# Kernel tuning notes

Hardware: AMD Instinct MI355X
Metric: run time of the kernel (lower is better)

## Reference

```python
import jax, jax.numpy as jnp
import numpy as np

N = 16384
K = 8

def knn_indices(pos, k):
    # squared pairwise distances via ||a||^2 + ||b||^2 - 2 a.b  -> [N, N]
    sq = jnp.sum(pos * pos, axis=-1)
    d = sq[:, None] + sq[None, :] - 2.0 * (pos @ pos.T)
    n = pos.shape[0]
    d = d.at[jnp.arange(n), jnp.arange(n)].set(jnp.inf)  # exclude self (loop=False)
    _, idx = jax.lax.top_k(-d, k)  # k nearest neighbors per target node
    # PointNetConv adds self-loops by default -> append self index
    return jnp.concatenate([idx, jnp.arange(n)[:, None]], axis=1)  # [N, k+1]

def mlp(x, W1, b1, W2, b2):
    return jax.nn.relu(x @ W1 + b1) @ W2 + b2

def pointnet_conv(x, pos, idx, W1, b1, W2, b2):
    # message: concat(x_j, pos_j - pos_i); aggregate: max over neighbors
    rel = pos[idx] - pos[:, None, :]                 # [N, k+1, 3]
    msg = jnp.concatenate([x[idx], rel], axis=-1)    # [N, k+1, d+3]
    h = mlp(msg, W1, b1, W2, b2)                     # [N, k+1, d_out]
    return jnp.max(h, axis=1)                        # [N, d_out]

def setup_inputs() -> dict:
    key = jax.random.key(0)
    ks = jax.random.split(key, 11)
    def lin(k, fi, fo):
        kw, kb = jax.random.split(k)
        s = 1.0 / np.sqrt(fi)
        return (jax.random.uniform(kw, (fi, fo), jnp.float32, -s, s),
                jax.random.uniform(kb, (fo,), jnp.float32, -s, s))
    W1a, b1a = lin(ks[0], 6, 32)
    W1b, b1b = lin(ks[1], 32, 64)
    W2a, b2a = lin(ks[2], 67, 64)
    W2b, b2b = lin(ks[3], 64, 128)
    Wc, bc = lin(ks[4], 128, 5)
    pos = jax.random.normal(ks[5], (N, 3), jnp.float32)
    return {"pos": pos, "W1a": W1a, "b1a": b1a, "W1b": W1b, "b1b": b1b,
            "W2a": W2a, "b2a": b2a, "W2b": W2b, "b2b": b2b, "Wc": Wc, "bc": bc}

def reference(pos, W1a, b1a, W1b, b1b, W2a, b2a, W2b, b2b, Wc, bc):
    idx = knn_indices(pos, K)                                    # [N, K+1]
    x = jax.nn.relu(pointnet_conv(pos, pos, idx, W1a, b1a, W1b, b1b))  # [N, 64]
    x = jax.nn.relu(pointnet_conv(x, pos, idx, W2a, b2a, W2b, b2b))    # [N, 128]
    logits = x @ Wc + bc                                         # [N, 5]
    return jax.nn.log_softmax(logits, axis=-1)
```

## Files before the change

kernel.cpp:

```cpp
#include <hip/hip_runtime.h>
#include <hip/hip_bf16.h>
#include <math.h>

#define N_PTS 16384
#define KNN 8

#define DT_BF16 1
#define DT_FP32 2

#define WS_FLAG_OFF 0
#define WS_IDX_OFF  64
#define WS_X1_OFF   589888
#define WS_NEEDED   4784192

#define WS_SAT_OFF      (WS_X1_OFF)
#define WS_START_OFF    (WS_X1_OFF + 442368)
#define WS_CURSOR_OFF   (WS_X1_OFF + 884800)
#define WS_PID_OFF      (WS_X1_OFF + 1327168)
#define WS_PTS_OFF      (WS_X1_OFF + 1392704)
#define WS_ROWTOT_OFF   (WS_X1_OFF + 1654848)
#define WS_ROWSTART_OFF (WS_X1_OFF + 1664064)
#define WS_XPRE_OFF     (WS_X1_OFF + 1673280)

#define GRID_R   48
#define NROWS2D  (GRID_R * GRID_R)
#define NCELLS   (GRID_R * GRID_R * GRID_R)
#define GLO      -4.5f
#define CELL_E   0.1875f
#define CELL_INV 5.3333335f
#define NBR_MIN  26
#define NBR_LO   9
#define M_CAP    768

__device__ __forceinline__ float bf2f(__hip_bfloat16 v) { return __bfloat162float(v); }

__device__ __forceinline__ float ldf(const float* p, int i) { return p[i]; }
__device__ __forceinline__ float ldf(const __hip_bfloat16* p, int i) { return bf2f(p[i]); }
__device__ __forceinline__ void stf(float* p, int i, float v) { p[i] = v; }
__device__ __forceinline__ void stf(__hip_bfloat16* p, int i, float v) { p[i] = __float2bfloat16(v); }

__device__ __forceinline__ int clamp_idx(int j) {
    return ((unsigned)j < (unsigned)N_PTS) ? j : 0;
}

__device__ __forceinline__ int cell_of(float v) {
    int c = (int)((v - GLO) * CELL_INV);
    return min(max(c, 0), GRID_R - 1);
}

__device__ __forceinline__ int get_dt(const int* flag) {
    return (flag[0] > 16) ? DT_FP32 : DT_BF16;
}

__global__ __launch_bounds__(256) void zero_kernel(int* __restrict__ cnt, int* __restrict__ flag) {
    const int e = blockIdx.x * 256 + threadIdx.x;
    cnt[e] = 0;
    if (e == 0) flag[0] = 0;
}

__global__ __launch_bounds__(256) void sniff_kernel(const unsigned short* __restrict__ posu,
                                                    int* __restrict__ flag) {
    __shared__ int red[256];
    int local = 0;
    for (int e = blockIdx.x * 256 + threadIdx.x; e < 3 * N_PTS; e += 64 * 256) {
        const float v = __uint_as_float(((unsigned)posu[e]) << 16);
        if (!(fabsf(v) <= 64.0f)) local++;
    }
    red[threadIdx.x] = local;
    __syncthreads();
    for (int s = 128; s > 0; s >>= 1) {
        if (threadIdx.x < s) red[threadIdx.x] += red[threadIdx.x + s];
        __syncthreads();
    }
    if (threadIdx.x == 0 && red[0] > 0) atomicAdd(flag, red[0]);
}

template <typename T>
__device__ __forceinline__ void count_body(const T* __restrict__ pos, int* __restrict__ cnt) {
    const int i = blockIdx.x * 256 + threadIdx.x;
    const float x = ldf(pos, 3 * i + 0);
    const float y = ldf(pos, 3 * i + 1);
    const float z = ldf(pos, 3 * i + 2);
    const int c = (cell_of(z) * GRID_R + cell_of(y)) * GRID_R + cell_of(x);
    atomicAdd(&cnt[c], 1);
}

__global__ __launch_bounds__(256) void grid_count_kernel(const void* __restrict__ pos,
                                                         const int* __restrict__ flag,
                                                         int* __restrict__ cnt) {
    if (get_dt(flag) == DT_BF16) count_body<__hip_bfloat16>((const __hip_bfloat16*)pos, cnt);
    else                         count_body<float>((const float*)pos, cnt);
}

__global__ __launch_bounds__(256) void rowscan_kernel(int* __restrict__ sat,
                                                      int* __restrict__ xpre,
                                                      int* __restrict__ rowtot) {
    const int t = blockIdx.x * 256 + threadIdx.x;
    const int rb = t * GRID_R;
    int acc = 0;
    for (int x = 0; x < GRID_R; ++x) {
        acc += sat[rb + x];
        sat[rb + x]  = acc;
        xpre[rb + x] = acc;
    }
    rowtot[t] = acc;
}

__global__ __launch_bounds__(256) void rowoffset_kernel(const int* __restrict__ rowtot,
                                                        int* __restrict__ rowstart) {
    __shared__ int part[256];
    const int t = threadIdx.x;
    int loc[9]; int s = 0;
#pragma unroll
    for (int k = 0; k < 9; ++k) { loc[k] = rowtot[t * 9 + k]; s += loc[k]; }
    part[t] = s;
    __syncthreads();
    for (int off = 1; off < 256; off <<= 1) {
        int v = (t >= off) ? part[t - off] : 0;
        __syncthreads();
        part[t] += v;
        __syncthreads();
    }
    int run = (t == 0) ? 0 : part[t - 1];
#pragma unroll
    for (int k = 0; k < 9; ++k) { rowstart[t * 9 + k] = run; run += loc[k]; }
}

__global__ __launch_bounds__(256) void cellsaty_kernel(const int* __restrict__ xpre,
                                                       const int* __restrict__ rowstart,
                                                       int* __restrict__ cstart,
                                                       int* __restrict__ cursor,
                                                       int* __restrict__ sat) {
    const int t = blockIdx.x * 256 + threadIdx.x;
    const int rb = t * GRID_R;
    const int base = rowstart[t];
    int prev = 0;
    for (int x = 0; x < GRID_R; ++x) {
        const int v = base + prev;
        cstart[rb + x] = v;
        cursor[rb + x] = v;
        prev = xpre[rb + x];
    }
    if (t == NROWS2D - 1) cstart[NCELLS] = base + prev;
    const int z = t / GRID_R, x = t - z * GRID_R;
    const int b2 = z * NROWS2D + x;
    int run = 0;
#pragma unroll
    for (int y = 0; y < GRID_R; ++y) {
        run += sat[b2 + y * GRID_R];
        sat[b2 + y * GRID_R] = run;
    }
}

template <typename T>
__device__ __forceinline__ void scatter_body(const T* __restrict__ pos, int i,
                                             int* __restrict__ cursor,
                                             float4* __restrict__ pts4, int* __restrict__ pid) {
    const float x = ldf(pos, 3 * i + 0);
    const float y = ldf(pos, 3 * i + 1);
    const float z = ldf(pos, 3 * i + 2);
    const int c = (cell_of(z) * GRID_R + cell_of(y)) * GRID_R + cell_of(x);
    const int slot = atomicAdd(&cursor[c], 1);
    const float sq = fmaf(x, x, fmaf(y, y, z * z));
    pts4[slot] = make_float4(-2.0f * x, -2.0f * y, -2.0f * z, sq);
    pid[slot] = i;
}

__global__ __launch_bounds__(256) void satzscatter_kernel(const void* __restrict__ pos,
                                                          const int* __restrict__ flag,
                                                          int* __restrict__ sat,
                                                          int* __restrict__ cursor,
                                                          float4* __restrict__ pts4,
                                                          int* __restrict__ pid) {
    if (blockIdx.x < 9) {
        const int t = blockIdx.x * 256 + threadIdx.x;
        int run = 0;
#pragma unroll
        for (int z = 0; z < GRID_R; ++z) {
            run += sat[t + z * NROWS2D];
            sat[t + z * NROWS2D] = run;
        }
    } else {
        const int i = (blockIdx.x - 9) * 256 + threadIdx.x;
        if (get_dt(flag) == DT_BF16) scatter_body<__hip_bfloat16>((const __hip_bfloat16*)pos, i, cursor, pts4, pid);
        else                         scatter_body<float>((const float*)pos, i, cursor, pts4, pid);
    }
}

__device__ __forceinline__ int sat_at(const int* __restrict__ sat, int x, int y, int z) {
    if (x < 0 || y < 0 || z < 0) return 0;
    return sat[(z * GRID_R + y) * GRID_R + x];
}

__device__ __forceinline__ int boxcount(const int* __restrict__ sat,
                                        int x0, int x1, int y0, int y1, int z0, int z1) {
    return sat_at(sat, x1, y1, z1) - sat_at(sat, x0 - 1, y1, z1)
         - sat_at(sat, x1, y0 - 1, z1) - sat_at(sat, x1, y1, z0 - 1)
         + sat_at(sat, x0 - 1, y0 - 1, z1) + sat_at(sat, x0 - 1, y1, z0 - 1)
         + sat_at(sat, x1, y0 - 1, z0 - 1) - sat_at(sat, x0 - 1, y0 - 1, z0 - 1);
}

template <typename T>
__device__ void knn_body(const T* __restrict__ pos,
                         const int* __restrict__ cstart, const int* __restrict__ sat,
                         const float4* __restrict__ pts4, const int* __restrict__ pid,
                         int* __restrict__ idx_out,
                         int* __restrict__ rs, int* __restrict__ epf) {
    const int tid  = threadIdx.x;
    const int lane = tid & 31;
    const int i    = blockIdx.x * 8 + (tid >> 5);

    const float pix = ldf(pos, 3 * i + 0);
    const float piy = ldf(pos, 3 * i + 1);
    const float piz = ldf(pos, 3 * i + 2);
    const float sqi = fmaf(pix, pix, fmaf(piy, piy, piz * piz));
    const int cx = cell_of(pix), cy = cell_of(piy), cz = cell_of(piz);

    float bd[KNN];
    int   bi[KNN];
#pragma unroll
    for (int q = 0; q < KNN; ++q) { bd[q] = INFINITY; bi[q] = 0x7fffffff; }
    float tau = INFINITY;

    auto do_insert = [&](float d, int pj) {
        float cd = d; int ci = pj;
#pragma unroll
        for (int q = 0; q < KNN; ++q) {
            const bool ins = (cd < bd[q]) || (cd == bd[q] && ci < bi[q]);
            const float nd = ins ? cd : bd[q];
            const int   ni = ins ? ci : bi[q];
            const float od = ins ? bd[q] : cd;
            const int   oi = ins ? bi[q] : ci;
            bd[q] = nd; bi[q] = ni; cd = od; ci = oi;
        }
        tau = fminf(tau, bd[KNN - 1]);
    };

    auto scan_win = [&](int rr) {
        const int x0 = max(cx - rr, 0), x1 = min(cx + rr, GRID_R - 1);
        const int y0 = max(cy - rr, 0), y1 = min(cy + rr, GRID_R - 1);
        const int z0 = max(cz - rr, 0), z1 = min(cz + rr, GRID_R - 1);
        const int ny = y1 - y0 + 1;
        const int R  = ny * (z1 - z0 + 1);
        const int xs = x1 - x0 + 1;
        for (int cb = 0; cb < R; cb += 32) {
            const int lr = cb + lane;
            int cnt_r = 0, st_r = 0;
            if (lr < R) {
                const int iz = lr / ny;
                const int iy = lr - iz * ny;
                const int c0 = ((z0 + iz) * GRID_R + (y0 + iy)) * GRID_R + x0;
                st_r  = cstart[c0];
                cnt_r = cstart[c0 + xs] - st_r;
            }
            int pv = cnt_r;
#pragma unroll
            for (int s = 1; s < 32; s <<= 1) {
                const int u = __shfl_up(pv, s, 32);
                if (lane >= s) pv += u;
            }
            const int Mtot = __shfl(pv, 31, 32);
            asm volatile("s_waitcnt lgkmcnt(0)" ::: "memory");
            rs[lane]  = st_r;
            epf[lane] = (lr < R) ? (pv - cnt_r) : 0x7fffffff;
            asm volatile("s_waitcnt lgkmcnt(0)" ::: "memory");
            for (int tb = 0; tb < Mtot; tb += 128) {
                float dls[4]; int pjs[4];
#pragma unroll
                for (int k = 0; k < 4; ++k) {
                    const int t = tb + (k << 5) + lane;
                    dls[k] = INFINITY; pjs[k] = i;
                    if (t < Mtot) {
                        int p = 0;
#pragma unroll
                        for (int st = 16; st >= 1; st >>= 1)
                            if (epf[p + st] <= t) p += st;
                        const int si = rs[p] + (t - epf[p]);
                        const float4 cq = pts4[si];
                        pjs[k] = pid[si];
                        dls[k] = fmaf(cq.x, pix, fmaf(cq.y, piy, fmaf(cq.z, piz, cq.w)));
                    }
                }
#pragma unroll
                for (int k = 0; k < 4; ++k)
                    if (pjs[k] != i && dls[k] <= tau) do_insert(dls[k], pjs[k]);
            }
        }
    };

    float od[KNN];
    int   oi[KNN];
    auto merge_out = [&]() {
#pragma unroll
        for (int k = 0; k < KNN; ++k) {
            float dw = bd[0];
            int   iw = bi[0];
#pragma unroll
            for (int s = 1; s < 32; s <<= 1) {
                const float dx = __shfl_xor(dw, s, 32);
                const int   ix = __shfl_xor(iw, s, 32);
                if (dx < dw || (dx == dw && ix < iw)) { dw = dx; iw = ix; }
            }
            if (bd[0] == dw && bi[0] == iw) {
#pragma unroll
                for (int q = 0; q < KNN - 1; ++q) { bd[q] = bd[q + 1]; bi[q] = bi[q + 1]; }
                bd[KNN - 1] = INFINITY; bi[KNN - 1] = 0x7fffffff;
            }
            od[k] = dw; oi[k] = iw;
        }
    };

    int r;
    {
        const int rl = lane + 1;
        const int bx0 = max(cx - rl, 0), bx1 = min(cx + rl, GRID_R - 1);
        const int by0 = max(cy - rl, 0), by1 = min(cy + rl, GRID_R - 1);
        const int bz0 = max(cz - rl, 0), bz1 = min(cz + rl, GRID_R - 1);
        const int cntl = boxcount(sat, bx0, bx1, by0, by1, bz0, bz1);
        const unsigned long long m9  = __ballot(cntl >= NBR_LO);
        const unsigned long long m26 = __ballot(cntl >= NBR_MIN);
        const unsigned sh  = (unsigned)(tid & 32);
        const unsigned mh9  = (unsigned)(m9  >> sh);
        const unsigned mh26 = (unsigned)(m26 >> sh);
        const int r9  = mh9  ? (int)__ffs(mh9)  : 32;
        const int r26 = mh26 ? (int)__ffs(mh26) : 32;
        const int cnt26 = __shfl(cntl, r26 - 1, 32);
        r = (cnt26 <= M_CAP) ? r26 : r9;
    }

    scan_win(r);

    {
        float mg = INFINITY;
        bool full = true;
        if (cx - r > 0)          { mg = fminf(mg, pix - (GLO + (float)(cx - r) * CELL_E));     full = false; }
        if (cx + r < GRID_R - 1) { mg = fminf(mg, (GLO + (float)(cx + r + 1) * CELL_E) - pix); full = false; }
        if (cy - r > 0)          { mg = fminf(mg, piy - (GLO + (float)(cy - r) * CELL_E));     full = false; }
        if (cy + r < GRID_R - 1) { mg = fminf(mg, (GLO + (float)(cy + r + 1) * CELL_E) - piy); full = false; }
        if (cz - r > 0)          { mg = fminf(mg, piz - (GLO + (float)(cz - r) * CELL_E));     full = false; }
        if (cz + r < GRID_R - 1) { mg = fminf(mg, (GLO + (float)(cz + r + 1) * CELL_E) - piz); full = false; }

        merge_out();
        bool done = full;
        const float d8 = od[KNN - 1];
        if (!full) {
            const float mge  = mg - 1e-5f;
            const float need = mge * mge - sqi;
            done = (d8 < need);
        }

        if (!done) {
            float s2 = sqrtf(fmaxf(d8 + sqi, 0.0f)) + 1e-4f;
            s2 = fminf(s2, 9.0f);
            auto dneed = [&](float frac, int clip) -> int {
                int nd = (int)ceilf((s2 - frac) * CELL_INV);
                nd = max(nd, 0);
                return min(nd, clip);
            };
            const float fxm = pix - (GLO + (float)cx * CELL_E);
            const float fxp = (GLO + (float)(cx + 1) * CELL_E) - pix;
            const float fym = piy - (GLO + (float)cy * CELL_E);
            const float fyp = (GLO + (float)(cy + 1) * CELL_E) - piy;
            const float fzm = piz - (GLO + (float)cz * CELL_E);
            const float fzp = (GLO + (float)(cz + 1) * CELL_E) - piz;
            int r2 = r + 1;
            r2 = max(r2, dneed(fxm, cx));
            r2 = max(r2, dneed(fxp, GRID_R - 1 - cx));
            r2 = max(r2, dneed(fym, cy));
            r2 = max(r2, dneed(fyp, GRID_R - 1 - cy));
            r2 = max(r2, dneed(fzm, cz));
            r2 = max(r2, dneed(fzp, GRID_R - 1 - cz));
            r2 = min(r2, GRID_R);

#pragma unroll
            for (int q = 0; q < KNN; ++q) { bd[q] = INFINITY; bi[q] = 0x7fffffff; }
            tau = d8;
            scan_win(r2);
            merge_out();
        }
    }

    if (lane == 0) {
#pragma unroll
        for (int k = 0; k < KNN; ++k) idx_out[i * 9 + k] = clamp_idx(oi[k]);
        idx_out[i * 9 + 8] = i;
    }
}

__global__ __launch_bounds__(256) void knn_grid_kernel(const void* __restrict__ pos,
                                                       const int* __restrict__ flag,
                                                       const int* __restrict__ cstart,
                                                       const int* __restrict__ sat,
                                                       const float4* __restrict__ pts4,
                                                       const int* __restrict__ pid,
                                                       int* __restrict__ idx_out) {
    __shared__ int rs[8][32];
    __shared__ int epf[8][32];
    const int sg = threadIdx.x >> 5;
    if (get_dt(flag) == DT_BF16)
        knn_body<__hip_bfloat16>((const __hip_bfloat16*)pos, cstart, sat, pts4, pid, idx_out,
                                 rs[sg], epf[sg]);
    else
        knn_body<float>((const float*)pos, cstart, sat, pts4, pid, idx_out, rs[sg], epf[sg]);
}

struct Conv1Smem {
    alignas(16) float wB[32 * 64];
    alignas(16) float h1s[4][9 * 32];
    alignas(16) float wsum[3 * 32];
    alignas(16) float wbot[3 * 32];
    alignas(16) float posn[4][9][3];
    float bA[32];
    float bB[64];
};

template <typename T>
__device__ void conv1_body(const T* __restrict__ pos, const int* __restrict__ idx,
                           const T* __restrict__ W1a, const T* __restrict__ b1a,
                           const T* __restrict__ W1b, const T* __restrict__ b1b,
                           float* __restrict__ x1, Conv1Smem& s) {
    const int tid = threadIdx.x;
    for (int e = tid; e < 96; e += 256) {
        const float bot = ldf(W1a, 96 + e);
        s.wsum[e] = ldf(W1a, e) + bot;
        s.wbot[e] = bot;
    }
    if (tid < 32) s.bA[tid] = ldf(b1a, tid);
    for (int e = tid; e < 2048; e += 256) s.wB[e] = ldf(W1b, e);
    if (tid < 64) s.bB[tid] = ldf(b1b, tid);

    const int tl   = tid >> 6;
    const int lane = tid & 63;
    const int i    = blockIdx.x * 4 + tl;

    if (lane < 27) {
        const int n = lane / 3, c = lane % 3;
        const int j = clamp_idx(idx[i * 9 + n]);
        s.posn[tl][n][c] = ldf(pos, 3 * j + c);
    }
    const float pi0 = ldf(pos, 3 * i + 0);
    const float pi1 = ldf(pos, 3 * i + 1);
    const float pi2 = ldf(pos, 3 * i + 2);
    __syncthreads();

    for (int e = lane; e < 288; e += 64) {
        const int n = e >> 5, k = e & 31;
        float b = fmaf(pi0, s.wbot[k], fmaf(pi1, s.wbot[32 + k], pi2 * s.wbot[64 + k]));
        float v = s.bA[k] - b;
        v = fmaf(s.posn[tl][n][0], s.wsum[k], v);
        v = fmaf(s.posn[tl][n][1], s.wsum[32 + k], v);
        v = fmaf(s.posn[tl][n][2], s.wsum[64 + k], v);
        s.h1s[tl][n * 32 + k] = fmaxf(v, 0.0f);
    }
    __syncthreads();

    float wcol[32];
#pragma unroll
    for (int k = 0; k < 32; ++k) wcol[k] = s.wB[k * 64 + lane];

    float acc = -INFINITY;
    for (int n = 0; n < 9; ++n) {
        float s0 = s.bB[lane], s1 = 0.0f, s2 = 0.0f, s3 = 0.0f;
#pragma unroll
        for (int k = 0; k < 32; k += 4) {
            s0 = fmaf(s.h1s[tl][n * 32 + k + 0], wcol[k + 0], s0);
            s1 = fmaf(s.h1s[tl][n * 32 + k + 1], wcol[k + 1], s1);
            s2 = fmaf(s.h1s[tl][n * 32 + k + 2], wcol[k + 2], s2);
            s3 = fmaf(s.h1s[tl][n * 32 + k + 3], wcol[k + 3], s3);
        }
        acc = fmaxf(acc, (s0 + s1) + (s2 + s3));
    }
    x1[i * 64 + lane] = fmaxf(acc, 0.0f);
}

__global__ __launch_bounds__(256) void conv1_kernel(const void* __restrict__ pos,
                                                    const int* __restrict__ flag,
                                                    const int* __restrict__ idx,
                                                    const void* __restrict__ W1a,
                                                    const void* __restrict__ b1a,
                                                    const void* __restrict__ W1b,
                                                    const void* __restrict__ b1b,
                                                    float* __restrict__ x1) {
    __shared__ Conv1Smem s;
    if (get_dt(flag) == DT_BF16)
        conv1_body<__hip_bfloat16>((const __hip_bfloat16*)pos, idx,
            (const __hip_bfloat16*)W1a, (const __hip_bfloat16*)b1a,
            (const __hip_bfloat16*)W1b, (const __hip_bfloat16*)b1b, x1, s);
    else
        conv1_body<float>((const float*)pos, idx, (const float*)W1a, (const float*)b1a,
            (const float*)W1b, (const float*)b1b, x1, s);
}

struct ZwSmem {
    alignas(16) float wA[67 * 64];
    alignas(16) float xrT[4][68][4];
    float bA[64];
};

template <typename T>
__device__ void zw_body(const T* __restrict__ pos, const T* __restrict__ W2a,
                        const T* __restrict__ b2a, float* __restrict__ x1, ZwSmem& s) {
    const int tid  = threadIdx.x;
    const int wv   = tid >> 6;
    const int lane = tid & 63;
    const int j0   = blockIdx.x * 16 + wv * 4;

    for (int e = tid; e < 4288; e += 256) s.wA[e] = ldf(W2a, e);
    if (tid < 64) s.bA[tid] = ldf(b2a, tid);

#pragma unroll
    for (int p = 0; p < 4; ++p)
        s.xrT[wv][lane][p] = x1[(j0 + p) * 64 + lane];
    if (lane < 12) {
        const int p = lane / 3, c = lane % 3;
        s.xrT[wv][64 + c][p] = ldf(pos, 3 * (j0 + p) + c);
    }
    __syncthreads();

    float a0 = s.bA[lane], a1 = a0, a2 = a0, a3 = a0;
    for (int c = 0; c < 67; ++c) {
        const float w = s.wA[c * 64 + lane];
        const float4 xv = *(const float4*)&s.xrT[wv][c][0];
        a0 = fmaf(xv.x, w, a0);
        a1 = fmaf(xv.y, w, a1);
        a2 = fmaf(xv.z, w, a2);
        a3 = fmaf(xv.w, w, a3);
    }
    x1[(j0 + 0) * 64 + lane] = a0;
    x1[(j0 + 1) * 64 + lane] = a1;
    x1[(j0 + 2) * 64 + lane] = a2;
    x1[(j0 + 3) * 64 + lane] = a3;
}

__global__ __launch_bounds__(256) void zw_kernel(const void* __restrict__ pos,
                                                 const int* __restrict__ flag,
                                                 const void* __restrict__ W2a,
                                                 const void* __restrict__ b2a,
                                                 float* __restrict__ x1) {
    __shared__ ZwSmem s;
    if (get_dt(flag) == DT_BF16)
        zw_body<__hip_bfloat16>((const __hip_bfloat16*)pos, (const __hip_bfloat16*)W2a,
                                (const __hip_bfloat16*)b2a, x1, s);
    else
        zw_body<float>((const float*)pos, (const float*)W2a, (const float*)b2a, x1, s);
}

struct Conv2Smem {
    alignas(16) float h1s[4][9 * 64];
    alignas(16) float row[4][128];
    alignas(16) float wbot[3 * 64];
    alignas(16) float wc[640];
    float bcs[5];
    float sv[4][5];
    int   nb[4][9];
};

template <typename T>
__device__ void conv2_body(const T* __restrict__ pos, const int* __restrict__ idx,
                           const float* __restrict__ zw,
                           const T* __restrict__ W2a, const T* __restrict__ W2b,
                           const T* __restrict__ b2b, const T* __restrict__ Wc,
                           const T* __restrict__ bc, T* __restrict__ out, Conv2Smem& s) {
    const int tid  = threadIdx.x;
    const int l    = tid & 127;
    const int half = tid >> 7;

    float wcol[64];
#pragma unroll
    for (int k = 0; k < 64; ++k) wcol[k] = ldf(W2b, k * 128 + l);
    const float bBl = ldf(b2b, l);

    for (int e = tid; e < 192; e += 256) s.wbot[e] = ldf(W2a, 4096 + e);
    for (int e = tid; e < 640; e += 256) s.wc[e] = ldf(Wc, e);
    if (tid < 5) s.bcs[tid] = ldf(bc, tid);

    const int tl   = tid >> 6;
    const int lane = tid & 63;
    const int i    = blockIdx.x * 4 + tl;

    if (lane < 9) s.nb[tl][lane] = clamp_idx(idx[i * 9 + lane]);
    const float pi0 = ldf(pos, 3 * i + 0);
    const float pi1 = ldf(pos, 3 * i + 1);
    const float pi2 = ldf(pos, 3 * i + 2);
    __syncthreads();

    {
        const float vi = fmaf(pi0, s.wbot[lane], fmaf(pi1, s.wbot[64 + lane], pi2 * s.wbot[128 + lane]));
#pragma unroll
        for (int n = 0; n < 9; ++n) {
            const int j = s.nb[tl][n];
            s.h1s[tl][n * 64 + lane] = fmaxf(zw[j * 64 + lane] - vi, 0.0f);
        }
    }
    __syncthreads();

#pragma unroll
    for (int tt = 0; tt < 2; ++tt) {
        const int tgt = half * 2 + tt;
        float acc = -INFINITY;
        for (int n = 0; n < 9; ++n) {
            float s0 = bBl, s1 = 0.0f, s2 = 0.0f, s3 = 0.0f;
#pragma unroll
            for (int k = 0; k < 64; k += 16) {
                const float4 h0 = *(const float4*)&s.h1s[tgt][n * 64 + k + 0];
                const float4 h1 = *(const float4*)&s.h1s[tgt][n * 64 + k + 4];
                const float4 h2 = *(const float4*)&s.h1s[tgt][n * 64 + k + 8];
                const float4 h3 = *(const float4*)&s.h1s[tgt][n * 64 + k + 12];
                s0 = fmaf(h0.x, wcol[k + 0], s0);
                s0 = fmaf(h0.y, wcol[k + 1], s0);
                s0 = fmaf(h0.z, wcol[k + 2], s0);
                s0 = fmaf(h0.w, wcol[k + 3], s0);
                s1 = fmaf(h1.x, wcol[k + 4], s1);
                s1 = fmaf(h1.y, wcol[k + 5], s1);
                s1 = fmaf(h1.z, wcol[k + 6], s1);
                s1 = fmaf(h1.w, wcol[k + 7], s1);
                s2 = fmaf(h2.x, wcol[k + 8], s2);
                s2 = fmaf(h2.y, wcol[k + 9], s2);
                s2 = fmaf(h2.z, wcol[k + 10], s2);
                s2 = fmaf(h2.w, wcol[k + 11], s2);
                s3 = fmaf(h3.x, wcol[k + 12], s3);
                s3 = fmaf(h3.y, wcol[k + 13], s3);
                s3 = fmaf(h3.z, wcol[k + 14], s3);
                s3 = fmaf(h3.w, wcol[k + 15], s3);
            }
            acc = fmaxf(acc, (s0 + s1) + (s2 + s3));
        }
        s.row[tgt][l] = fmaxf(acc, 0.0f);
    }
    __syncthreads();

    if (tid < 20) {
        const int tgt = tid / 5, o = tid % 5;
        float v = s.bcs[o];
        for (int k = 0; k < 128; ++k) v = fmaf(s.row[tgt][k], s.wc[k * 5 + o], v);
        s.sv[tgt][o] = v;
    }
    __syncthreads();
    if (tid < 20) {
        const int tgt = tid / 5, o = tid % 5;
        float m = s.sv[tgt][0];
#pragma unroll
        for (int q = 1; q < 5; ++q) m = fmaxf(m, s.sv[tgt][q]);
        float sum = 0.0f;
#pragma unroll
        for (int q = 0; q < 5; ++q) sum += expf(s.sv[tgt][q] - m);
        const float lse = m + logf(sum);
        stf(out, (blockIdx.x * 4 + tgt) * 5 + o, s.sv[tgt][o] - lse);
    }
}

__global__ __launch_bounds__(256) void conv2_head_kernel(const void* __restrict__ pos,
                                                         const int* __restrict__ flag,
                                                         const int* __restrict__ idx,
                                                         const float* __restrict__ zw,
                                                         const void* __restrict__ W2a,
                                                         const void* __restrict__ W2b,
                                                         const void* __restrict__ b2b,
                                                         const void* __restrict__ Wc,
                                                         const void* __restrict__ bc,
                                                         void* __restrict__ out) {
    __shared__ Conv2Smem s;
    if (get_dt(flag) == DT_BF16)
        conv2_body<__hip_bfloat16>((const __hip_bfloat16*)pos, idx, zw,
            (const __hip_bfloat16*)W2a, (const __hip_bfloat16*)W2b, (const __hip_bfloat16*)b2b,
            (const __hip_bfloat16*)Wc, (const __hip_bfloat16*)bc, (__hip_bfloat16*)out, s);
    else
        conv2_body<float>((const float*)pos, idx, zw, (const float*)W2a, (const float*)W2b,
            (const float*)b2b, (const float*)Wc, (const float*)bc, (float*)out, s);
}

extern "C" void kernel_launch(void* const* d_in, const int* in_sizes, int n_in,
                              void* d_out, int out_size, void* d_ws, size_t ws_size,
                              hipStream_t stream) {
    if (ws_size < (size_t)WS_NEEDED) return;

    char* ws = (char*)d_ws;
    int*    flag     = (int*)(ws + WS_FLAG_OFF);
    int*    idx      = (int*)(ws + WS_IDX_OFF);
    float*  x1       = (float*)(ws + WS_X1_OFF);
    int*    sat      = (int*)(ws + WS_SAT_OFF);
    int*    cstart   = (int*)(ws + WS_START_OFF);
    int*    cursor   = (int*)(ws + WS_CURSOR_OFF);
    int*    pid      = (int*)(ws + WS_PID_OFF);
    float4* pts4     = (float4*)(ws + WS_PTS_OFF);
    int*    rowtot   = (int*)(ws + WS_ROWTOT_OFF);
    int*    rowstart = (int*)(ws + WS_ROWSTART_OFF);
    int*    xpre     = (int*)(ws + WS_XPRE_OFF);

    zero_kernel<<<NCELLS / 256, 256, 0, stream>>>(sat, flag);
    sniff_kernel<<<64, 256, 0, stream>>>((const unsigned short*)d_in[0], flag);
    grid_count_kernel<<<N_PTS / 256, 256, 0, stream>>>(d_in[0], flag, sat);
    rowscan_kernel<<<NROWS2D / 256, 256, 0, stream>>>(sat, xpre, rowtot);
    rowoffset_kernel<<<1, 256, 0, stream>>>(rowtot, rowstart);
    cellsaty_kernel<<<NROWS2D / 256, 256, 0, stream>>>(xpre, rowstart, cstart, cursor, sat);
    satzscatter_kernel<<<9 + N_PTS / 256, 256, 0, stream>>>(d_in[0], flag, sat, cursor, pts4, pid);
    knn_grid_kernel<<<N_PTS / 8, 256, 0, stream>>>(d_in[0], flag, cstart, sat, pts4, pid, idx);
    conv1_kernel<<<N_PTS / 4, 256, 0, stream>>>(d_in[0], flag, idx,
        d_in[1], d_in[2], d_in[3], d_in[4], x1);
    zw_kernel<<<N_PTS / 16, 256, 0, stream>>>(d_in[0], flag, d_in[5], d_in[6], x1);
    conv2_head_kernel<<<N_PTS / 4, 256, 0, stream>>>(d_in[0], flag, idx, x1,
        d_in[5], d_in[7], d_in[8], d_in[9], d_in[10], d_out);
}
```

Baseline: 241.6 us.

## Restructure conv MLP loops to reuse weights across neighbors and tune grid search caps

The second-layer MLP loops in conv1 and conv2 now iterate over k-tiles outermost, keeping 9 per-neighbor accumulators in registers. Each weight is loaded once per tile and applied to all neighbors, instead of holding a full weight column in registers. The bias add is hoisted out of the max, which is valid because the bias is the same for every neighbor. In conv2 each wave now handles its own target and both output halves, replacing the split of 128 lanes across two targets. Weights are read from global memory inside the loop rather than preloaded. The KNN grid constants NBR_MIN and M_CAP are also raised, which changes candidate-search coverage and cost.

```diff
diff --git a/kernel.cpp b/kernel.cpp
--- a/kernel.cpp
+++ b/kernel.cpp
@@ -28,9 +28,9 @@
 #define GLO      -4.5f
 #define CELL_E   0.1875f
 #define CELL_INV 5.3333335f
-#define NBR_MIN  26
+#define NBR_MIN  40
 #define NBR_LO   9
-#define M_CAP    768
+#define M_CAP    1024
 
 __device__ __forceinline__ float bf2f(__hip_bfloat16 v) { return __bfloat162float(v); }
 
@@ -454,23 +454,35 @@
     }
     __syncthreads();
 
-    float wcol[32];
-#pragma unroll
-    for (int k = 0; k < 32; ++k) wcol[k] = s.wB[k * 64 + lane];
-
-    float acc = -INFINITY;
-    for (int n = 0; n < 9; ++n) {
-        float s0 = s.bB[lane], s1 = 0.0f, s2 = 0.0f, s3 = 0.0f;
-#pragma unroll
-        for (int k = 0; k < 32; k += 4) {
-            s0 = fmaf(s.h1s[tl][n * 32 + k + 0], wcol[k + 0], s0);
-            s1 = fmaf(s.h1s[tl][n * 32 + k + 1], wcol[k + 1], s1);
-            s2 = fmaf(s.h1s[tl][n * 32 + k + 2], wcol[k + 2], s2);
-            s3 = fmaf(s.h1s[tl][n * 32 + k + 3], wcol[k + 3], s3);
-        }
-        acc = fmaxf(acc, (s0 + s1) + (s2 + s3));
-    }
-    x1[i * 64 + lane] = fmaxf(acc, 0.0f);
+    float acc[9];
+#pragma unroll
+    for (int n = 0; n < 9; ++n) acc[n] = 0.0f;
+#pragma unroll
+    for (int kt = 0; kt < 32; kt += 8) {
+        float w0 = s.wB[(kt + 0) * 64 + lane];
+        float w1 = s.wB[(kt + 1) * 64 + lane];
+        float w2 = s.wB[(kt + 2) * 64 + lane];
+        float w3 = s.wB[(kt + 3) * 64 + lane];
+        float w4 = s.wB[(kt + 4) * 64 + lane];
+        float w5 = s.wB[(kt + 5) * 64 + lane];
+        float w6 = s.wB[(kt + 6) * 64 + lane];
+        float w7 = s.wB[(kt + 7) * 64 + lane];
+#pragma unroll
+        for (int n = 0; n < 9; ++n) {
+            const float4 ha = *(const float4*)&s.h1s[tl][n * 32 + kt];
+            const float4 hb = *(const float4*)&s.h1s[tl][n * 32 + kt + 4];
+            float a = acc[n];
+            a = fmaf(ha.x, w0, a); a = fmaf(ha.y, w1, a);
+            a = fmaf(ha.z, w2, a); a = fmaf(ha.w, w3, a);
+            a = fmaf(hb.x, w4, a); a = fmaf(hb.y, w5, a);
+            a = fmaf(hb.z, w6, a); a = fmaf(hb.w, w7, a);
+            acc[n] = a;
+        }
+    }
+    float m = acc[0];
+#pragma unroll
+    for (int n = 1; n < 9; ++n) m = fmaxf(m, acc[n]);
+    x1[i * 64 + lane] = fmaxf(m + s.bB[lane], 0.0f);
 }
 
 __global__ __launch_bounds__(256) void conv1_kernel(const void* __restrict__ pos,
@@ -562,21 +574,13 @@
                            const T* __restrict__ b2b, const T* __restrict__ Wc,
                            const T* __restrict__ bc, T* __restrict__ out, Conv2Smem& s) {
     const int tid  = threadIdx.x;
-    const int l    = tid & 127;
-    const int half = tid >> 7;
-
-    float wcol[64];
-#pragma unroll
-    for (int k = 0; k < 64; ++k) wcol[k] = ldf(W2b, k * 128 + l);
-    const float bBl = ldf(b2b, l);
+    const int tl   = tid >> 6;
+    const int lane = tid & 63;
+    const int i    = blockIdx.x * 4 + tl;
 
     for (int e = tid; e < 192; e += 256) s.wbot[e] = ldf(W2a, 4096 + e);
     for (int e = tid; e < 640; e += 256) s.wc[e] = ldf(Wc, e);
     if (tid < 5) s.bcs[tid] = ldf(bc, tid);
-
-    const int tl   = tid >> 6;
-    const int lane = tid & 63;
-    const int i    = blockIdx.x * 4 + tl;
 
     if (lane < 9) s.nb[tl][lane] = clamp_idx(idx[i * 9 + lane]);
     const float pi0 = ldf(pos, 3 * i + 0);
@@ -594,39 +598,35 @@
     }
     __syncthreads();
 
-#pragma unroll
-    for (int tt = 0; tt < 2; ++tt) {
-        const int tgt = half * 2 + tt;
-        float acc = -INFINITY;
+    float acc0[9], acc1[9];
+#pragma unroll
+    for (int n = 0; n < 9; ++n) { acc0[n] = 0.0f; acc1[n] = 0.0f; }
+#pragma unroll
+    for (int kt = 0; kt < 64; kt += 4) {
+        const float wa0 = ldf(W2b, (kt + 0) * 128 + lane);
+        const float wa1 = ldf(W2b, (kt + 1) * 128 + lane);
+        const float wa2 = ldf(W2b, (kt + 2) * 128 + lane);
+        const float wa3 = ldf(W2b, (kt + 3) * 128 + lane);
+        const float wb0 = ldf(W2b, (kt + 0) * 128 + lane + 64);
+        const float wb1 = ldf(W2b, (kt + 1) * 128 + lane + 64);
+        const float wb2 = ldf(W2b, (kt + 2) * 128 + lane + 64);
+        const float wb3 = ldf(W2b, (kt + 3) * 128 + lane + 64);
+#pragma unroll
         for (int n = 0; n < 9; ++n) {
-            float s0 = bBl, s1 = 0.0f, s2 = 0.0f, s3 = 0.0f;
-#pragma unroll
-            for (int k = 0; k < 64; k += 16) {
-                const float4 h0 = *(const float4*)&s.h1s[tgt][n * 64 + k + 0];
-                const float4 h1 = *(const float4*)&s.h1s[tgt][n * 64 + k + 4];
-                const float4 h2 = *(const float4*)&s.h1s[tgt][n * 64 + k + 8];
-                const float4 h3 = *(const float4*)&s.h1s[tgt][n * 64 + k + 12];
-                s0 = fmaf(h0.x, wcol[k + 0], s0);
-                s0 = fmaf(h0.y, wcol[k + 1], s0);
-                s0 = fmaf(h0.z, wcol[k + 2], s0);
-                s0 = fmaf(h0.w, wcol[k + 3], s0);
-                s1 = fmaf(h1.x, wcol[k + 4], s1);
-                s1 = fmaf(h1.y, wcol[k + 5], s1);
-                s1 = fmaf(h1.z, wcol[k + 6], s1);
-                s1 = fmaf(h1.w, wcol[k + 7], s1);
-                s2 = fmaf(h2.x, wcol[k + 8], s2);
-                s2 = fmaf(h2.y, wcol[k + 9], s2);
-                s2 = fmaf(h2.z, wcol[k + 10], s2);
-                s2 = fmaf(h2.w, wcol[k + 11], s2);
-                s3 = fmaf(h3.x, wcol[k + 12], s3);
-                s3 = fmaf(h3.y, wcol[k + 13], s3);
-                s3 = fmaf(h3.z, wcol[k + 14], s3);
-                s3 = fmaf(h3.w, wcol[k + 15], s3);
-            }
-            acc = fmaxf(acc, (s0 + s1) + (s2 + s3));
-        }
-        s.row[tgt][l] = fmaxf(acc, 0.0f);
-    }
+            const float4 h = *(const float4*)&s.h1s[tl][n * 64 + kt];
+            float a0 = acc0[n], a1 = acc1[n];
+            a0 = fmaf(h.x, wa0, a0); a0 = fmaf(h.y, wa1, a0);
+            a0 = fmaf(h.z, wa2, a0); a0 = fmaf(h.w, wa3, a0);
+            a1 = fmaf(h.x, wb0, a1); a1 = fmaf(h.y, wb1, a1);
+            a1 = fmaf(h.z, wb2, a1); a1 = fmaf(h.w, wb3, a1);
+            acc0[n] = a0; acc1[n] = a1;
+        }
+    }
+    float m0 = acc0[0], m1 = acc1[0];
+#pragma unroll
+    for (int n = 1; n < 9; ++n) { m0 = fmaxf(m0, acc0[n]); m1 = fmaxf(m1, acc1[n]); }
+    s.row[tl][lane]      = fmaxf(m0 + ldf(b2b, lane), 0.0f);
+    s.row[tl][lane + 64] = fmaxf(m1 + ldf(b2b, lane + 64), 0.0f);
     __syncthreads();
 
     if (tid < 20) {
```

New measurement: 235.4 us. 1.03x faster.
